# Performance work log

Hardware: AMD Instinct MI355X
Metric: run time of the kernel (lower is better)

Reference implementation:

```python
import jax, jax.numpy as jnp
import numpy as np

DIM = 192
HEADS = 8
EPS = 1e-12  # torch F.normalize eps


def _l2norm(t):
    # normalize over last axis, matching torch.nn.functional.normalize
    n = jnp.sqrt(jnp.sum(t * t, axis=-1, keepdims=True))
    return t / jnp.maximum(n, EPS)


def setup_inputs() -> dict:
    key = jax.random.key(0)
    k1, k2, k3, k4 = jax.random.split(key, 4)
    B, C, H, W = 16, DIM, 128, 128
    s = 1.0 / np.sqrt(C)
    return {
        "x": jax.random.normal(k1, (B, C, H, W), dtype=jnp.float32),
        "w_qkv": jax.random.normal(k2, (C, 3 * C), dtype=jnp.float32) * s,
        "w_proj": jax.random.normal(k3, (C, C), dtype=jnp.float32) * s,
        "b_proj": jax.random.normal(k4, (C,), dtype=jnp.float32) * 0.01,
        "temperature": jnp.ones((HEADS, 1, 1), dtype=jnp.float32),
    }


def reference(x, w_qkv, w_proj, b_proj, temperature):
    B, C, H, W = x.shape
    N = H * W
    h = HEADS
    d = C // h
    # [B,C,H,W] -> [B,N,C]
    xt = x.reshape(B, C, N).transpose(0, 2, 1)
    qkv = (xt @ w_qkv).reshape(B, N, 3, h, d)
    qkv = qkv.transpose(2, 0, 3, 1, 4)           # [3,B,h,N,d]
    q, k, v = qkv[0], qkv[1], qkv[2]
    # transpose to channel-as-token: [B,h,d,N]
    q = _l2norm(q.transpose(0, 1, 3, 2))
    k = _l2norm(k.transpose(0, 1, 3, 2))
    v = v.transpose(0, 1, 3, 2)
    # small channel attention matrix [B,h,d,d]
    attn = jnp.einsum("bhdn,bhen->bhde", q, k) * temperature
    attn = jax.nn.softmax(attn, axis=-1)
    out = jnp.einsum("bhde,bhen->bhdn", attn, v)  # [B,h,d,N]
    out = out.transpose(0, 3, 1, 2).reshape(B, N, C)
    out = out @ w_proj + b_proj
    return out.transpose(0, 2, 1).reshape(B, C, H, W)
```

## Files before the change

### kernel.cpp

```cpp
#include <hip/hip_runtime.h>
#include <hip/hip_bf16.h>
#include <math.h>

#define C_DIM 192
#define NTOK 16384
#define NB 16
#define NH 8
#define HD 24
#define EPSN 1e-12f

typedef float f32x4 __attribute__((ext_vector_type(4)));
typedef __bf16 bf16x4 __attribute__((ext_vector_type(4)));
typedef __bf16 bf16x8 __attribute__((ext_vector_type(8)));

__device__ __forceinline__ f32x4 mfma16(bf16x8 a, bf16x8 b, f32x4 c) {
  return __builtin_amdgcn_mfma_f32_16x16x32_bf16(a, b, c, 0, 0, 0);
}

__device__ __forceinline__ bf16x8 cvt8(const float* __restrict__ p) {
  f32x4 a = *(const f32x4*)p;
  f32x4 b = *(const f32x4*)(p + 4);
  bf16x8 r;
  r[0] = (__bf16)a[0]; r[1] = (__bf16)a[1]; r[2] = (__bf16)a[2]; r[3] = (__bf16)a[3];
  r[4] = (__bf16)b[0]; r[5] = (__bf16)b[1]; r[6] = (__bf16)b[2]; r[7] = (__bf16)b[3];
  return r;
}

__global__ __launch_bounds__(256, 2) void k1_gram(const float* __restrict__ x,
                                                  float* __restrict__ gpart,
                                                  int kc) {
  const int b = blockIdx.y, chunk = blockIdx.x;
  const float* xb = x + (size_t)b * C_DIM * NTOK + (size_t)chunk * kc;
  __shared__ __bf16 xsh[2][C_DIM * 40];
  const int t = threadIdx.x;
  const int lane = t & 63, wid = t >> 6;
  const int lrow = lane & 15, loct = lane >> 4;
  const int r0 = (wid >> 1) * 96, c0 = (wid & 1) * 96;
  f32x4 acc[6][6] = {};
  f32x4 sA[6], sB[6];
  const int nst = kc >> 5;

#define K1_LOADR(dst, ks)                                                      \
  {                                                                            \
    _Pragma("unroll") for (int it = 0; it < 6; ++it) {                         \
      int idx = it * 256 + t, r = idx >> 3, c8 = idx & 7;                      \
      dst[it] = *(const f32x4*)(xb + (size_t)r * NTOK + (ks) + 4 * c8);        \
    }                                                                          \
  }
#define K1_STORE(buf, src)                                                     \
  {                                                                            \
    _Pragma("unroll") for (int it = 0; it < 6; ++it) {                         \
      int idx = it * 256 + t, r = idx >> 3, c8 = idx & 7;                      \
      bf16x4 w;                                                                \
      w[0] = (__bf16)src[it][0]; w[1] = (__bf16)src[it][1];                    \
      w[2] = (__bf16)src[it][2]; w[3] = (__bf16)src[it][3];                    \
      *(bf16x4*)(&xsh[buf][r * 40 + 4 * c8]) = w;                              \
    }                                                                          \
  }
#define K1_COMP(buf)                                                           \
  {                                                                            \
    bf16x8 fa[6];                                                              \
    _Pragma("unroll") for (int i = 0; i < 6; ++i)                              \
        fa[i] = *(const bf16x8*)(&xsh[buf][(r0 + 16 * i + lrow) * 40 +         \
                                           8 * loct]);                         \
    _Pragma("unroll") for (int j = 0; j < 6; ++j) {                            \
      bf16x8 fb =                                                              \
          *(const bf16x8*)(&xsh[buf][(c0 + 16 * j + lrow) * 40 + 8 * loct]);   \
      _Pragma("unroll") for (int i = 0; i < 6; ++i)                            \
          acc[i][j] = mfma16(fa[i], fb, acc[i][j]);                            \
    }                                                                          \
  }

  K1_LOADR(sA, 0);
  K1_STORE(0, sA);
  K1_LOADR(sB, 32);
  __syncthreads();

  for (int s = 0; s < nst; s += 2) {
    if (s + 2 < nst) K1_LOADR(sA, 32 * (s + 2));
    K1_COMP(0);
    K1_STORE(1, sB);
    __syncthreads();
    if (s + 3 < nst) K1_LOADR(sB, 32 * (s + 3));
    K1_COMP(1);
    if (s + 2 < nst) K1_STORE(0, sA);
    __syncthreads();
  }
#undef K1_LOADR
#undef K1_STORE
#undef K1_COMP

  float* gp = gpart + ((size_t)chunk * NB + b) * C_DIM * C_DIM;
#pragma unroll
  for (int i = 0; i < 6; ++i)
#pragma unroll
    for (int j = 0; j < 6; ++j)
#pragma unroll
      for (int e = 0; e < 4; ++e)
        gp[(size_t)(r0 + 16 * i + 4 * loct + e) * C_DIM + (c0 + 16 * j + lrow)] =
            acc[i][j][e];
}

__global__ __launch_bounds__(256) void k2a_reduce(const float* __restrict__ gpart,
                                                  float* __restrict__ G,
                                                  int nchunk) {
  const size_t total = (size_t)NB * C_DIM * C_DIM;
  size_t e0 = ((size_t)blockIdx.x * 256 + threadIdx.x) * 4;
  f32x4 s = {};
  for (int c = 0; c < nchunk; ++c) s += *(const f32x4*)(gpart + c * total + e0);
  *(f32x4*)(G + e0) = s;
}

__global__ __launch_bounds__(256) void k2b1_t(const float* __restrict__ G,
                                              const float* __restrict__ wqkv,
                                              float* __restrict__ Tt) {
  const int b = blockIdx.y, rb = blockIdx.x;
  const int lane = threadIdx.x & 63, wid = threadIdx.x >> 6;
  const int lrow = lane & 15, loct = lane >> 4;
  const float* Gb = G + (size_t)b * C_DIM * C_DIM;
  const int ddA = rb * 64 + wid * 16 + lrow;
  f32x4 acc[12] = {};
  for (int s = 0; s < 6; ++s) {
    bf16x8 fa;
#pragma unroll
    for (int e = 0; e < 8; ++e)
      fa[e] = (__bf16)wqkv[(size_t)(32 * s + 8 * loct + e) * 576 + ddA];
#pragma unroll
    for (int j = 0; j < 12; ++j) {
      bf16x8 fb = cvt8(Gb + (size_t)(16 * j + lrow) * C_DIM + 32 * s + 8 * loct);
      acc[j] = mfma16(fa, fb, acc[j]);
    }
  }
  float* To = Tt + (size_t)b * 384 * C_DIM;
#pragma unroll
  for (int j = 0; j < 12; ++j)
#pragma unroll
    for (int e = 0; e < 4; ++e)
      To[(size_t)(rb * 64 + wid * 16 + 4 * loct + e) * C_DIM + 16 * j + lrow] =
          acc[j][e];
}

__global__ __launch_bounds__(256) void k2b2_attn(const float* __restrict__ Tt,
                                                 const float* __restrict__ wqkv,
                                                 const float* __restrict__ temp,
                                                 float* __restrict__ Yt) {
  const int b = blockIdx.y, h = blockIdx.x;
  __shared__ float SL[32][33];
  __shared__ float qn2L[HD], kn2L[HD];
  const int t = threadIdx.x;
  const int lane = t & 63, wid = t >> 6;
  const int lrow = lane & 15, loct = lane >> 4;
  const float* Tb = Tt + (size_t)b * 384 * C_DIM;
  const int r = wid >> 1, j = wid & 1;
  f32x4 acc = {};
  for (int s = 0; s < 6; ++s) {
    bf16x8 fa = cvt8(Tb + (size_t)(h * HD + 16 * r + lrow) * C_DIM + 32 * s + 8 * loct);
    bf16x8 fb;
#pragma unroll
    for (int e = 0; e < 8; ++e)
      fb[e] = (__bf16)wqkv[(size_t)(32 * s + 8 * loct + e) * 576 + 192 + h * HD +
                           16 * j + lrow];
    acc = mfma16(fa, fb, acc);
  }
#pragma unroll
  for (int e = 0; e < 4; ++e) {
    int d = 16 * r + 4 * loct + e, ee = 16 * j + lrow;
    if (d < HD && ee < HD) SL[d][ee] = acc[e];
  }
  if (t < 48) {
    const int dd = (t < 24) ? t : t - 24;
    const int row = ((t < 24) ? 0 : 192) + h * HD + dd;
    float s = 0.f;
    for (int c = 0; c < C_DIM; ++c)
      s += Tb[(size_t)row * C_DIM + c] * wqkv[(size_t)c * 576 + row];
    if (t < 24) qn2L[dd] = s; else kn2L[dd] = s;
  }
  __syncthreads();
  if (t < HD) {
    const float tp = temp[h];
    float nq = fmaxf(sqrtf(fmaxf(qn2L[t], 0.f)), EPSN);
    float lg[HD];
    float m = -1e30f;
#pragma unroll
    for (int e = 0; e < HD; ++e) {
      float nk = fmaxf(sqrtf(fmaxf(kn2L[e], 0.f)), EPSN);
      lg[e] = SL[t][e] / (nq * nk) * tp;
      m = fmaxf(m, lg[e]);
    }
    float sum = 0.f;
#pragma unroll
    for (int e = 0; e < HD; ++e) { lg[e] = __expf(lg[e] - m); sum += lg[e]; }
    float inv = 1.f / sum;
#pragma unroll
    for (int e = 0; e < HD; ++e) SL[t][e] = lg[e] * inv;
  }
  __syncthreads();
  if (t < C_DIM) {
    float wv[HD];
#pragma unroll
    for (int e = 0; e < HD; ++e)
      wv[e] = wqkv[(size_t)t * 576 + 384 + h * HD + e];
    float* Yo = Yt + ((size_t)b * C_DIM + t) * C_DIM + h * HD;
#pragma unroll
    for (int d = 0; d < HD; ++d) {
      float y = 0.f;
#pragma unroll
      for (int e = 0; e < HD; ++e) y += SL[d][e] * wv[e];
      Yo[d] = y;
    }
  }
}

__global__ __launch_bounds__(256) void k2c_m(const float* __restrict__ wproj,
                                             const float* __restrict__ Yt,
                                             __bf16* __restrict__ M) {
  const int b = blockIdx.y, rb = blockIdx.x;
  const int lane = threadIdx.x & 63, wid = threadIdx.x >> 6;
  const int lrow = lane & 15, loct = lane >> 4;
  const float* Yb = Yt + (size_t)b * C_DIM * C_DIM;
  const int coA = rb * 64 + wid * 16 + lrow;
  f32x4 acc[12] = {};
  for (int s = 0; s < 6; ++s) {
    bf16x8 fa;
#pragma unroll
    for (int e = 0; e < 8; ++e)
      fa[e] = (__bf16)wproj[(size_t)(32 * s + 8 * loct + e) * C_DIM + coA];
#pragma unroll
    for (int j = 0; j < 12; ++j) {
      bf16x8 fb = cvt8(Yb + (size_t)(16 * j + lrow) * C_DIM + 32 * s + 8 * loct);
      acc[j] = mfma16(fa, fb, acc[j]);
    }
  }
  __bf16* Mo = M + (size_t)b * C_DIM * C_DIM;
#pragma unroll
  for (int j = 0; j < 12; ++j)
#pragma unroll
    for (int e = 0; e < 4; ++e)
      Mo[(size_t)(rb * 64 + wid * 16 + 4 * loct + e) * C_DIM + 16 * j + lrow] =
          (__bf16)acc[j][e];
}

__global__ __launch_bounds__(256, 3) void k3_out(const float* __restrict__ x,
                                                 const __bf16* __restrict__ M,
                                                 const float* __restrict__ bproj,
                                                 float* __restrict__ out) {
  const int nt = blockIdx.x, half = blockIdx.y, b = blockIdx.z;
  const int rbase = half * 96;
  __shared__ __bf16 Ml[96 * C_DIM];
  __shared__ float biasL[96];
  const int t = threadIdx.x;
  const int lane = t & 63, w = t >> 6;
  const int lrow = lane & 15, loct = lane >> 4;

  const __bf16* Mb = M + (size_t)b * C_DIM * C_DIM + (size_t)rbase * C_DIM;
  for (int i = t; i < 96 * 24; i += 256) {
    int row = i / 24, ch = i % 24;
    bf16x8 v = *(const bf16x8*)(Mb + row * C_DIM + ch * 8);
    *(bf16x8*)(Ml + row * C_DIM + ((ch ^ (row & 7)) * 8)) = v;
  }
  if (t < 96) biasL[t] = bproj[rbase + t];
  __syncthreads();

  const float* xb = x + (size_t)b * C_DIM * NTOK;
  float* ob = out + (size_t)b * C_DIM * NTOK;
  const int n0 = nt * 256 + w * 64;

  f32x4 acc[6][4] = {};
  f32x4 xs4[8];
#pragma unroll
  for (int e = 0; e < 8; ++e)
    xs4[e] = *(const f32x4*)(xb + (size_t)(8 * loct + e) * NTOK + n0 + 4 * lrow);

  for (int s = 0; s < 6; ++s) {
    bf16x8 fb[4];
#pragma unroll
    for (int nf = 0; nf < 4; ++nf)
#pragma unroll
      for (int e = 0; e < 8; ++e)
        fb[nf][e] = (__bf16)xs4[e][nf];
    if (s < 5) {
#pragma unroll
      for (int e = 0; e < 8; ++e)
        xs4[e] = *(const f32x4*)(xb + (size_t)(32 * (s + 1) + 8 * loct + e) * NTOK +
                                 n0 + 4 * lrow);
    }
#pragma unroll
    for (int tt = 0; tt < 6; ++tt) {
      int rowb = 16 * tt + lrow;
      bf16x8 fa = *(const bf16x8*)(Ml + rowb * C_DIM +
                                   (((4 * s + loct) ^ (rowb & 7)) * 8));
#pragma unroll
      for (int nf = 0; nf < 4; ++nf)
        acc[tt][nf] = mfma16(fa, fb[nf], acc[tt][nf]);
    }
  }

  __syncthreads();
  float* epi_w = (float*)Ml + w * 1088;
#pragma unroll
  for (int tt = 0; tt < 6; ++tt) {
    f32x4 bias4 = *(const f32x4*)(biasL + 16 * tt + 4 * loct);
#pragma unroll
    for (int e = 0; e < 4; ++e) {
      f32x4 v;
      v[0] = acc[tt][0][e] + bias4[e];
      v[1] = acc[tt][1][e] + bias4[e];
      v[2] = acc[tt][2][e] + bias4[e];
      v[3] = acc[tt][3][e] + bias4[e];
      *(f32x4*)(epi_w + (4 * loct + e) * 68 + 4 * lrow) = v;
    }
#pragma unroll
    for (int h = 0; h < 4; ++h) {
      int r = 4 * h + loct;
      f32x4 v = *(const f32x4*)(epi_w + r * 68 + 4 * lrow);
      *(f32x4*)(ob + (size_t)(rbase + 16 * tt + r) * NTOK + n0 + 4 * lrow) = v;
    }
  }
}

extern "C" void kernel_launch(void* const* d_in, const int* in_sizes, int n_in,
                              void* d_out, int out_size, void* d_ws, size_t ws_size,
                              hipStream_t stream) {
  const float* x = (const float*)d_in[0];
  const float* wqkv = (const float*)d_in[1];
  const float* wproj = (const float*)d_in[2];
  const float* bproj = (const float*)d_in[3];
  const float* temp = (const float*)d_in[4];
  float* out = (float*)d_out;

  const size_t GSZ = (size_t)NB * C_DIM * C_DIM;
  const size_t TSZ = (size_t)NB * 384 * C_DIM;
  int nchunk = 32;
  while (nchunk > 1 &&
         ((size_t)nchunk * GSZ + GSZ + TSZ + GSZ + GSZ) * 4 > ws_size)
    nchunk >>= 1;
  float* wsf = (float*)d_ws;
  float* gpart = wsf;
  float* G = gpart + (size_t)nchunk * GSZ;
  float* Tt = G + GSZ;
  float* Yt = Tt + TSZ;
  __bf16* M = (__bf16*)(Yt + GSZ);

  k1_gram<<<dim3(nchunk, NB), 256, 0, stream>>>(x, gpart, NTOK / nchunk);
  k2a_reduce<<<dim3(576), 256, 0, stream>>>(gpart, G, nchunk);
  k2b1_t<<<dim3(6, NB), 256, 0, stream>>>(G, wqkv, Tt);
  k2b2_attn<<<dim3(NH, NB), 256, 0, stream>>>(Tt, wqkv, temp, Yt);
  k2c_m<<<dim3(3, NB), 256, 0, stream>>>(wproj, Yt, M);
  k3_out<<<dim3(NTOK / 256, 2, NB), 256, 0, stream>>>(x, M, bproj, out);
}
```

Baseline: 226.9 us.

## Load Gram-kernel MFMA fragments directly from global memory, dropping LDS staging

```diff
diff --git a/kernel.cpp b/kernel.cpp
--- a/kernel.cpp
+++ b/kernel.cpp
@@ -31,64 +31,37 @@
                                                   int kc) {
   const int b = blockIdx.y, chunk = blockIdx.x;
   const float* xb = x + (size_t)b * C_DIM * NTOK + (size_t)chunk * kc;
-  __shared__ __bf16 xsh[2][C_DIM * 40];
-  const int t = threadIdx.x;
-  const int lane = t & 63, wid = t >> 6;
+  const int lane = threadIdx.x & 63, wid = threadIdx.x >> 6;
   const int lrow = lane & 15, loct = lane >> 4;
   const int r0 = (wid >> 1) * 96, c0 = (wid & 1) * 96;
+  const float* pA = xb + (size_t)(r0 + lrow) * NTOK + 8 * loct;
+  const float* pB = xb + (size_t)(c0 + lrow) * NTOK + 8 * loct;
   f32x4 acc[6][6] = {};
-  f32x4 sA[6], sB[6];
-  const int nst = kc >> 5;
-
-#define K1_LOADR(dst, ks)                                                      \
+  bf16x8 fa0[6], fb0[6], fa1[6], fb1[6];
+
+#define K1_LOAD(fa_, fb_, ks)                                                  \
   {                                                                            \
-    _Pragma("unroll") for (int it = 0; it < 6; ++it) {                         \
-      int idx = it * 256 + t, r = idx >> 3, c8 = idx & 7;                      \
-      dst[it] = *(const f32x4*)(xb + (size_t)r * NTOK + (ks) + 4 * c8);        \
-    }                                                                          \
-  }
-#define K1_STORE(buf, src)                                                     \
+    _Pragma("unroll") for (int i = 0; i < 6; ++i)                              \
+        fa_[i] = cvt8(pA + (size_t)(16 * i) * NTOK + (ks));                    \
+    _Pragma("unroll") for (int j = 0; j < 6; ++j)                              \
+        fb_[j] = cvt8(pB + (size_t)(16 * j) * NTOK + (ks));                    \
+  }
+#define K1_MFMA(fa_, fb_)                                                      \
   {                                                                            \
-    _Pragma("unroll") for (int it = 0; it < 6; ++it) {                         \
-      int idx = it * 256 + t, r = idx >> 3, c8 = idx & 7;                      \
-      bf16x4 w;                                                                \
-      w[0] = (__bf16)src[it][0]; w[1] = (__bf16)src[it][1];                    \
-      w[2] = (__bf16)src[it][2]; w[3] = (__bf16)src[it][3];                    \
-      *(bf16x4*)(&xsh[buf][r * 40 + 4 * c8]) = w;                              \
-    }                                                                          \
-  }
-#define K1_COMP(buf)                                                           \
-  {                                                                            \
-    bf16x8 fa[6];                                                              \
-    _Pragma("unroll") for (int i = 0; i < 6; ++i)                              \
-        fa[i] = *(const bf16x8*)(&xsh[buf][(r0 + 16 * i + lrow) * 40 +         \
-                                           8 * loct]);                         \
-    _Pragma("unroll") for (int j = 0; j < 6; ++j) {                            \
-      bf16x8 fb =                                                              \
-          *(const bf16x8*)(&xsh[buf][(c0 + 16 * j + lrow) * 40 + 8 * loct]);   \
-      _Pragma("unroll") for (int i = 0; i < 6; ++i)                            \
-          acc[i][j] = mfma16(fa[i], fb, acc[i][j]);                            \
-    }                                                                          \
-  }
-
-  K1_LOADR(sA, 0);
-  K1_STORE(0, sA);
-  K1_LOADR(sB, 32);
-  __syncthreads();
-
-  for (int s = 0; s < nst; s += 2) {
-    if (s + 2 < nst) K1_LOADR(sA, 32 * (s + 2));
-    K1_COMP(0);
-    K1_STORE(1, sB);
-    __syncthreads();
-    if (s + 3 < nst) K1_LOADR(sB, 32 * (s + 3));
-    K1_COMP(1);
-    if (s + 2 < nst) K1_STORE(0, sA);
-    __syncthreads();
-  }
-#undef K1_LOADR
-#undef K1_STORE
-#undef K1_COMP
+    _Pragma("unroll") for (int j = 0; j < 6; ++j)                              \
+        _Pragma("unroll") for (int i = 0; i < 6; ++i)                          \
+            acc[i][j] = mfma16(fa_[i], fb_[j], acc[i][j]);                     \
+  }
+
+  K1_LOAD(fa0, fb0, 0);
+  for (int ks = 0; ks < kc; ks += 64) {
+    if (ks + 32 < kc) K1_LOAD(fa1, fb1, ks + 32);
+    K1_MFMA(fa0, fb0);
+    if (ks + 64 < kc) K1_LOAD(fa0, fb0, ks + 64);
+    K1_MFMA(fa1, fb1);
+  }
+#undef K1_LOAD
+#undef K1_MFMA
 
   float* gp = gpart + ((size_t)chunk * NB + b) * C_DIM * C_DIM;
 #pragma unroll
```

After: 393.6 us. 1.74x slower.

## Emit token-major bf16 copy of x from gram kernel for output GEMM

Applied to the files above, without the earlier changes.

```diff
diff --git a/kernel.cpp b/kernel.cpp
--- a/kernel.cpp
+++ b/kernel.cpp
@@ -28,33 +28,50 @@
 
 __global__ __launch_bounds__(256, 2) void k1_gram(const float* __restrict__ x,
                                                   float* __restrict__ gpart,
+                                                  __bf16* __restrict__ xe,
                                                   int kc) {
   const int b = blockIdx.y, chunk = blockIdx.x;
   const float* xb = x + (size_t)b * C_DIM * NTOK + (size_t)chunk * kc;
   __shared__ __bf16 xsh[2][C_DIM * 40];
+  __shared__ __bf16 tb[2][32 * C_DIM];
   const int t = threadIdx.x;
   const int lane = t & 63, wid = t >> 6;
   const int lrow = lane & 15, loct = lane >> 4;
   const int r0 = (wid >> 1) * 96, c0 = (wid & 1) * 96;
+  const int etok = t >> 3, eseg = t & 7;
+  __bf16* xe_b = xe + ((size_t)b * NTOK + (size_t)chunk * kc) * C_DIM;
   f32x4 acc[6][6] = {};
-  f32x4 sA[6], sB[6];
-  const int nst = kc >> 5;
-
-#define K1_LOADR(dst, ks)                                                      \
+  f32x4 stg[6];
+
+#define K1_LOADR(ks_)                                                          \
   {                                                                            \
     _Pragma("unroll") for (int it = 0; it < 6; ++it) {                         \
       int idx = it * 256 + t, r = idx >> 3, c8 = idx & 7;                      \
-      dst[it] = *(const f32x4*)(xb + (size_t)r * NTOK + (ks) + 4 * c8);        \
+      stg[it] = *(const f32x4*)(xb + (size_t)r * NTOK + (ks_) + 4 * c8);       \
     }                                                                          \
   }
-#define K1_STORE(buf, src)                                                     \
+#define K1_WRITE(buf)                                                          \
   {                                                                            \
     _Pragma("unroll") for (int it = 0; it < 6; ++it) {                         \
       int idx = it * 256 + t, r = idx >> 3, c8 = idx & 7;                      \
       bf16x4 w;                                                                \
-      w[0] = (__bf16)src[it][0]; w[1] = (__bf16)src[it][1];                    \
-      w[2] = (__bf16)src[it][2]; w[3] = (__bf16)src[it][3];                    \
+      w[0] = (__bf16)stg[it][0]; w[1] = (__bf16)stg[it][1];                    \
+      w[2] = (__bf16)stg[it][2]; w[3] = (__bf16)stg[it][3];                    \
       *(bf16x4*)(&xsh[buf][r * 40 + 4 * c8]) = w;                              \
+      _Pragma("unroll") for (int jj = 0; jj < 4; ++jj) {                       \
+        int tok = 4 * c8 + jj;                                                 \
+        tb[buf][tok * C_DIM + ((((r >> 3) ^ (tok & 7)) << 3) | (r & 7))] =     \
+            w[jj];                                                             \
+      }                                                                        \
+    }                                                                          \
+  }
+#define K1_EMIT(buf, ks_)                                                      \
+  {                                                                            \
+    _Pragma("unroll") for (int j = 0; j < 3; ++j) {                            \
+      int chk = 3 * eseg + j;                                                  \
+      bf16x8 v = *(const bf16x8*)&tb[buf][etok * C_DIM +                       \
+                                          ((chk ^ (etok & 7)) << 3)];          \
+      *(bf16x8*)(xe_b + (size_t)((ks_) + etok) * C_DIM + chk * 8) = v;         \
     }                                                                          \
   }
 #define K1_COMP(buf)                                                           \
@@ -71,23 +88,22 @@
     }                                                                          \
   }
 
-  K1_LOADR(sA, 0);
-  K1_STORE(0, sA);
-  K1_LOADR(sB, 32);
-  __syncthreads();
-
-  for (int s = 0; s < nst; s += 2) {
-    if (s + 2 < nst) K1_LOADR(sA, 32 * (s + 2));
-    K1_COMP(0);
-    K1_STORE(1, sB);
+  K1_LOADR(0);
+  K1_WRITE(0);
+  __syncthreads();
+
+  for (int ks = 0; ks < kc; ks += 32) {
+    const int cur = (ks >> 5) & 1;
+    const bool more = (ks + 32) < kc;
+    if (more) K1_LOADR(ks + 32);
+    K1_EMIT(cur, ks);
+    K1_COMP(cur);
+    if (more) K1_WRITE(cur ^ 1);
     __syncthreads();
-    if (s + 3 < nst) K1_LOADR(sB, 32 * (s + 3));
-    K1_COMP(1);
-    if (s + 2 < nst) K1_STORE(0, sA);
-    __syncthreads();
   }
 #undef K1_LOADR
-#undef K1_STORE
+#undef K1_WRITE
+#undef K1_EMIT
 #undef K1_COMP
 
   float* gp = gpart + ((size_t)chunk * NB + b) * C_DIM * C_DIM;
@@ -240,7 +256,7 @@
           (__bf16)acc[j][e];
 }
 
-__global__ __launch_bounds__(256, 3) void k3_out(const float* __restrict__ x,
+__global__ __launch_bounds__(256, 3) void k3_out(const __bf16* __restrict__ xe,
                                                  const __bf16* __restrict__ M,
                                                  const float* __restrict__ bproj,
                                                  float* __restrict__ out) {
@@ -261,28 +277,26 @@
   if (t < 96) biasL[t] = bproj[rbase + t];
   __syncthreads();
 
-  const float* xb = x + (size_t)b * C_DIM * NTOK;
+  const __bf16* xeb = xe + (size_t)b * NTOK * C_DIM;
   float* ob = out + (size_t)b * C_DIM * NTOK;
   const int n0 = nt * 256 + w * 64;
 
   f32x4 acc[6][4] = {};
-  f32x4 xs4[8];
-#pragma unroll
-  for (int e = 0; e < 8; ++e)
-    xs4[e] = *(const f32x4*)(xb + (size_t)(8 * loct + e) * NTOK + n0 + 4 * lrow);
+  bf16x8 xs8[4];
+#pragma unroll
+  for (int nf = 0; nf < 4; ++nf)
+    xs8[nf] = *(const bf16x8*)(xeb + (size_t)(n0 + 4 * lrow + nf) * C_DIM +
+                               8 * loct);
 
   for (int s = 0; s < 6; ++s) {
     bf16x8 fb[4];
 #pragma unroll
-    for (int nf = 0; nf < 4; ++nf)
-#pragma unroll
-      for (int e = 0; e < 8; ++e)
-        fb[nf][e] = (__bf16)xs4[e][nf];
+    for (int nf = 0; nf < 4; ++nf) fb[nf] = xs8[nf];
     if (s < 5) {
 #pragma unroll
-      for (int e = 0; e < 8; ++e)
-        xs4[e] = *(const f32x4*)(xb + (size_t)(32 * (s + 1) + 8 * loct + e) * NTOK +
-                                 n0 + 4 * lrow);
+      for (int nf = 0; nf < 4; ++nf)
+        xs8[nf] = *(const bf16x8*)(xeb + (size_t)(n0 + 4 * lrow + nf) * C_DIM +
+                                   32 * (s + 1) + 8 * loct);
     }
 #pragma unroll
     for (int tt = 0; tt < 6; ++tt) {
@@ -328,23 +342,25 @@
   const float* temp = (const float*)d_in[4];
   float* out = (float*)d_out;
 
+  const size_t XB = (size_t)NB * NTOK * C_DIM;
   const size_t GSZ = (size_t)NB * C_DIM * C_DIM;
   const size_t TSZ = (size_t)NB * 384 * C_DIM;
   int nchunk = 32;
   while (nchunk > 1 &&
-         ((size_t)nchunk * GSZ + GSZ + TSZ + GSZ + GSZ) * 4 > ws_size)
+         XB * 2 + ((size_t)nchunk * GSZ + GSZ + TSZ + GSZ + GSZ) * 4 > ws_size)
     nchunk >>= 1;
-  float* wsf = (float*)d_ws;
+  __bf16* xe = (__bf16*)d_ws;
+  float* wsf = (float*)d_ws + XB / 2;
   float* gpart = wsf;
   float* G = gpart + (size_t)nchunk * GSZ;
   float* Tt = G + GSZ;
   float* Yt = Tt + TSZ;
   __bf16* M = (__bf16*)(Yt + GSZ);
 
-  k1_gram<<<dim3(nchunk, NB), 256, 0, stream>>>(x, gpart, NTOK / nchunk);
+  k1_gram<<<dim3(nchunk, NB), 256, 0, stream>>>(x, gpart, xe, NTOK / nchunk);
   k2a_reduce<<<dim3(576), 256, 0, stream>>>(gpart, G, nchunk);
   k2b1_t<<<dim3(6, NB), 256, 0, stream>>>(G, wqkv, Tt);
   k2b2_attn<<<dim3(NH, NB), 256, 0, stream>>>(Tt, wqkv, temp, Yt);
   k2c_m<<<dim3(3, NB), 256, 0, stream>>>(wproj, Yt, M);
-  k3_out<<<dim3(NTOK / 256, 2, NB), 256, 0, stream>>>(x, M, bproj, out);
-}
+  k3_out<<<dim3(NTOK / 256, 2, NB), 256, 0, stream>>>(xe, M, bproj, out);
+}
```

Result: slower. 262.3 us (+15.6%).
